# Kernel optimization log

Measured on AMD Instinct MI355X. Metric: run time of the kernel, lower is better.

## Reference

```python
import jax, jax.numpy as jnp
import numpy as np

N = 50000      # node_num
DIN = 128      # input_dim
DH = 128       # hidden_dim
DE = 128       # embedding_dim
DD = 128       # decoder_dim
NE = 800000    # num edges (before self loops)
B = 4096       # drug pairs
EPS = 1e-5


def setup_inputs() -> dict:
    key = jax.random.key(0)
    ks = jax.random.split(key, 16)
    x = jax.random.normal(ks[0], (N, DIN), jnp.float32)
    edge_index = jax.random.randint(ks[1], (2, NE), 0, N, dtype=jnp.int32)
    drug_index = jax.random.randint(ks[2], (B, 2), 0, N, dtype=jnp.int32)
    s = 0.05  # weight scale for numerical sanity
    return {
        "x": x,
        "edge_index": edge_index,
        "drug_index": drug_index,
        "w1": jax.random.normal(ks[3], (DIN, DH), jnp.float32) * s,
        "b1": jnp.zeros((DH,), jnp.float32),
        "w2": jax.random.normal(ks[4], (DH, DH), jnp.float32) * s,
        "b2": jnp.zeros((DH,), jnp.float32),
        "w3": jax.random.normal(ks[5], (DH, DE), jnp.float32) * s,
        "b3": jnp.zeros((DE,), jnp.float32),
        "g1": jnp.ones((DH,), jnp.float32), "be1": jnp.zeros((DH,), jnp.float32),
        "g2": jnp.ones((DH,), jnp.float32), "be2": jnp.zeros((DH,), jnp.float32),
        "g3": jnp.ones((DE,), jnp.float32), "be3": jnp.zeros((DE,), jnp.float32),
        "p1": jax.random.normal(ks[6], (DE, DD), jnp.float32) * s,
        "p2": jax.random.normal(ks[7], (DD, DD), jnp.float32) * s,
    }


def gcn_conv(x, row, col, W, b):
    # row/col already include self loops; PyG: message from row (source), aggregated at col (target)
    n = x.shape[0]
    h = x @ W + b                                   # linear first, as in GCNConv.forward
    deg = jnp.zeros((n,), h.dtype).at[col].add(1.0)  # degree(col) incl. self loops -> >= 1
    dis = deg ** -0.5
    norm = dis[row] * dis[col]                      # [E+N]
    msg = norm[:, None] * h[row]                    # [E+N, d] gather
    return jax.ops.segment_sum(msg, col, num_segments=n)  # scatter-add


def batch_norm(x, gamma, beta):
    m = jnp.mean(x, axis=0)
    v = jnp.mean((x - m) ** 2, axis=0)  # biased var, as torch BatchNorm training
    return (x - m) * jax.lax.rsqrt(v + EPS) * gamma + beta


def leaky(x):
    return jnp.where(x >= 0, x, 0.1 * x)  # LeakyReLU(0.1)


def reference(x, edge_index, drug_index, w1, b1, w2, b2, w3, b3,
              g1, be1, g2, be2, g3, be3, p1, p2):
    n = x.shape[0]
    self_loop = jnp.arange(n, dtype=edge_index.dtype)
    row = jnp.concatenate([edge_index[0], self_loop])
    col = jnp.concatenate([edge_index[1], self_loop])

    h = leaky(batch_norm(gcn_conv(x, row, col, w1, b1), g1, be1))
    h = leaky(batch_norm(gcn_conv(h, row, col, w2, b2), g2, be2))
    h = leaky(batch_norm(gcn_conv(h, row, col, w3, b3), g3, be3))

    di = drug_index.reshape(-1, 2)
    a = h[di[:, 0] - 1]  # [B, DE] (1-based indices; -1 wraps like torch negative index)
    bb = h[di[:, 1] - 1]  # [B, DE]
    t = a @ p1 @ p2 @ p1.T            # [B, DE] bilinear decode, batched
    ypred = jnp.sum(t * bb, axis=1, keepdims=True)  # [B, 1]
    return ypred
```

## Files before the change

kernel.cpp:

```cpp
#include <hip/hip_runtime.h>

#define PAD 64
#define NSLOT 64

__global__ void init_kernel(int* __restrict__ cnt, int n) {
  int i = blockIdx.x * blockDim.x + threadIdx.x;
  int stride = gridDim.x * blockDim.x;
  for (int j = i; j < n; j += stride) cnt[j] = 0;
}

__global__ void fillcsr_kernel(const int* __restrict__ row, const int* __restrict__ col,
                               int* __restrict__ cnt, int* __restrict__ csr, int ne,
                               float* __restrict__ stats, int nstat) {
  int gid = blockIdx.x * blockDim.x + threadIdx.x;
  int stride = gridDim.x * blockDim.x;
  for (int j = gid; j < nstat; j += stride) stats[j] = 0.f;
  if (gid < ne) {
    int d = col[gid];
    int p = atomicAdd(&cnt[d], 1);
    if (p < PAD) csr[d * PAD + p] = row[gid];
  }
}

__global__ __launch_bounds__(256, 4) void gemm_kernel(
    const float* __restrict__ A, const float* __restrict__ W, const float* __restrict__ bias,
    float* __restrict__ out, int n, float invN,
    const float* __restrict__ bn_sum, const float* __restrict__ bn_sq,
    const float* __restrict__ bn_g, const float* __restrict__ bn_b, int use_bn,
    const int* __restrict__ cnt) {
  __shared__ float Ws[32 * 128];
  __shared__ float xs[32 * 128];
  __shared__ float bnsc[128], bnsh[128];
  int tid = threadIdx.x;
  if (tid < 128) {
    if (use_bn) {
      float s = 0.f, q = 0.f;
      for (int r2 = 0; r2 < NSLOT; ++r2) { s += bn_sum[r2 * 128 + tid]; q += bn_sq[r2 * 128 + tid]; }
      float m = s * invN;
      float var = q * invN - m * m;
      float rs = rsqrtf(var + 1e-5f);
      float sc = rs * bn_g[tid];
      bnsc[tid] = sc;
      bnsh[tid] = bn_b[tid] - m * sc;
    } else {
      bnsc[tid] = 1.f; bnsh[tid] = 0.f;
    }
  }
  int base = blockIdx.x * 128;
  int tx = tid & 15, ty = tid >> 4;
  int c0 = tx * 4, r0 = ty * 4;
  int r = tid & 127;
  int row_s = base + r;
  int hf = tid >> 7;
  int kw = tid >> 5;
  int c4 = tid & 31;
  const float4* Arow = (const float4*)(A + (size_t)row_s * 128);
  float acc[8][8];
#pragma unroll
  for (int i = 0; i < 8; ++i)
#pragma unroll
    for (int j = 0; j < 8; ++j) acc[i][j] = 0.f;

  for (int kp = 0; kp < 4; ++kp) {
    __syncthreads();
#pragma unroll
    for (int it = 0; it < 4; ++it) {
      int kl = kw + it * 8;
      float4 wv = ((const float4*)(W + (size_t)(kp * 32 + kl) * 128))[c4];
      *(float4*)&Ws[kl * 128 + c4 * 4] = wv;
    }
#pragma unroll
    for (int it = 0; it < 4; ++it) {
      int kbl = hf + it * 2;
      float4 v = make_float4(0.f, 0.f, 0.f, 0.f);
      if (row_s < n) v = Arow[kp * 8 + kbl];
      if (use_bn) {
        int k0 = kp * 32 + kbl * 4;
        float t;
        t = v.x * bnsc[k0 + 0] + bnsh[k0 + 0]; v.x = t >= 0.f ? t : 0.1f * t;
        t = v.y * bnsc[k0 + 1] + bnsh[k0 + 1]; v.y = t >= 0.f ? t : 0.1f * t;
        t = v.z * bnsc[k0 + 2] + bnsh[k0 + 2]; v.z = t >= 0.f ? t : 0.1f * t;
        t = v.w * bnsc[k0 + 3] + bnsh[k0 + 3]; v.w = t >= 0.f ? t : 0.1f * t;
      }
      int kl = kbl * 4;
      xs[(kl + 0) * 128 + r] = v.x;
      xs[(kl + 1) * 128 + r] = v.y;
      xs[(kl + 2) * 128 + r] = v.z;
      xs[(kl + 3) * 128 + r] = v.w;
    }
    __syncthreads();
#pragma unroll 4
    for (int k = 0; k < 32; ++k) {
      float4 a0 = *(const float4*)&xs[k * 128 + r0];
      float4 a1 = *(const float4*)&xs[k * 128 + 64 + r0];
      float4 w0 = *(const float4*)&Ws[k * 128 + c0];
      float4 w1 = *(const float4*)&Ws[k * 128 + 64 + c0];
      float xr[8], wc[8];
      xr[0] = a0.x; xr[1] = a0.y; xr[2] = a0.z; xr[3] = a0.w;
      xr[4] = a1.x; xr[5] = a1.y; xr[6] = a1.z; xr[7] = a1.w;
      wc[0] = w0.x; wc[1] = w0.y; wc[2] = w0.z; wc[3] = w0.w;
      wc[4] = w1.x; wc[5] = w1.y; wc[6] = w1.z; wc[7] = w1.w;
#pragma unroll
      for (int i = 0; i < 8; ++i)
#pragma unroll
        for (int j = 0; j < 8; ++j)
          acc[i][j] = fmaf(xr[i], wc[j], acc[i][j]);
    }
  }
  float bb0[4], bb1[4];
#pragma unroll
  for (int j = 0; j < 4; ++j) { bb0[j] = bias[c0 + j]; bb1[j] = bias[64 + c0 + j]; }
#pragma unroll
  for (int i = 0; i < 8; ++i) {
    int row = base + (i < 4 ? r0 + i : 64 + r0 + (i - 4));
    if (row < n) {
      float rs = rsqrtf((float)(cnt[row] + 1));
      float4 o0, o1;
      o0.x = (acc[i][0] + bb0[0]) * rs; o0.y = (acc[i][1] + bb0[1]) * rs;
      o0.z = (acc[i][2] + bb0[2]) * rs; o0.w = (acc[i][3] + bb0[3]) * rs;
      o1.x = (acc[i][4] + bb1[0]) * rs; o1.y = (acc[i][5] + bb1[1]) * rs;
      o1.z = (acc[i][6] + bb1[2]) * rs; o1.w = (acc[i][7] + bb1[3]) * rs;
      *(float4*)&out[(size_t)row * 128 + c0] = o0;
      *(float4*)&out[(size_t)row * 128 + 64 + c0] = o1;
    }
  }
}

__global__ __launch_bounds__(256) void agg_kernel(const float* __restrict__ z,
                                                  const int* __restrict__ cnt,
                                                  const int* __restrict__ csr,
                                                  float* __restrict__ out,
                                                  float* __restrict__ Ssum,
                                                  float* __restrict__ Ssq,
                                                  int n, int half) {
  __shared__ float bs[4][128], bq[4][128];
  int tid = threadIdx.x;
  int lane = tid & 63;
  int wv = tid >> 6;
  int w = (blockIdx.x * blockDim.x + tid) >> 6;
  float stx = 0.f, sty = 0.f, qtx = 0.f, qty = 0.f;
  if (w < half) {
    int i0 = w, i1 = w + half;
    bool has1 = (i1 < n);
    const float2* __restrict__ h2 = (const float2*)z;
    unsigned off0 = (unsigned)i0 * 64u + (unsigned)lane;
    unsigned off1 = (unsigned)i1 * 64u + (unsigned)lane;
    float2 self0 = h2[off0];
    float2 self1 = has1 ? h2[off1] : make_float2(0.f, 0.f);
    int c0r = cnt[i0];
    int c1r = has1 ? cnt[i1] : 0;
    float d0 = rsqrtf((float)(c0r + 1));
    float d1 = rsqrtf((float)(c1r + 1));
    int e0 = c0r > PAD ? PAD : c0r;
    int e1 = c1r > PAD ? PAD : c1r;
    const int* __restrict__ lp0 = csr + (size_t)i0 * PAD;
    const int* __restrict__ lp1 = csr + (size_t)i1 * PAD;
    float s0x = self0.x, s0y = self0.y;
    float s1x = self1.x, s1y = self1.y;
    int my0 = (lane < e0) ? lp0[lane] : 0;
    int my1 = (lane < e1) ? lp1[lane] : 0;
    int p0 = 0, p1 = 0;
    while (p0 + 8 <= e0 && p1 + 8 <= e1) {
      float2 v0[8], v1[8];
#pragma unroll
      for (int u = 0; u < 8; ++u) { int s = __shfl(my0, p0 + u, 64); v0[u] = h2[(unsigned)s * 64u + (unsigned)lane]; }
#pragma unroll
      for (int u = 0; u < 8; ++u) { int s = __shfl(my1, p1 + u, 64); v1[u] = h2[(unsigned)s * 64u + (unsigned)lane]; }
#pragma unroll
      for (int u = 0; u < 8; ++u) {
        s0x += v0[u].x; s0y += v0[u].y;
        s1x += v1[u].x; s1y += v1[u].y;
      }
      p0 += 8; p1 += 8;
    }
    for (; p0 + 8 <= e0; p0 += 8) {
      float2 v[8];
#pragma unroll
      for (int u = 0; u < 8; ++u) { int s = __shfl(my0, p0 + u, 64); v[u] = h2[(unsigned)s * 64u + (unsigned)lane]; }
#pragma unroll
      for (int u = 0; u < 8; ++u) { s0x += v[u].x; s0y += v[u].y; }
    }
    for (; p0 + 4 <= e0; p0 += 4) {
      float2 v[4];
#pragma unroll
      for (int u = 0; u < 4; ++u) { int s = __shfl(my0, p0 + u, 64); v[u] = h2[(unsigned)s * 64u + (unsigned)lane]; }
#pragma unroll
      for (int u = 0; u < 4; ++u) { s0x += v[u].x; s0y += v[u].y; }
    }
    for (; p0 < e0; ++p0) {
      int s = __shfl(my0, p0, 64);
      float2 v = h2[(unsigned)s * 64u + (unsigned)lane];
      s0x += v.x; s0y += v.y;
    }
    for (; p1 + 8 <= e1; p1 += 8) {
      float2 v[8];
#pragma unroll
      for (int u = 0; u < 8; ++u) { int s = __shfl(my1, p1 + u, 64); v[u] = h2[(unsigned)s * 64u + (unsigned)lane]; }
#pragma unroll
      for (int u = 0; u < 8; ++u) { s1x += v[u].x; s1y += v[u].y; }
    }
    for (; p1 + 4 <= e1; p1 += 4) {
      float2 v[4];
#pragma unroll
      for (int u = 0; u < 4; ++u) { int s = __shfl(my1, p1 + u, 64); v[u] = h2[(unsigned)s * 64u + (unsigned)lane]; }
#pragma unroll
      for (int u = 0; u < 4; ++u) { s1x += v[u].x; s1y += v[u].y; }
    }
    for (; p1 < e1; ++p1) {
      int s = __shfl(my1, p1, 64);
      float2 v = h2[(unsigned)s * 64u + (unsigned)lane];
      s1x += v.x; s1y += v.y;
    }
    float2 o0; o0.x = d0 * s0x; o0.y = d0 * s0y;
    ((float2*)out)[off0] = o0;
    stx += o0.x; qtx = fmaf(o0.x, o0.x, qtx);
    sty += o0.y; qty = fmaf(o0.y, o0.y, qty);
    if (has1) {
      float2 o1; o1.x = d1 * s1x; o1.y = d1 * s1y;
      ((float2*)out)[off1] = o1;
      stx += o1.x; qtx = fmaf(o1.x, o1.x, qtx);
      sty += o1.y; qty = fmaf(o1.y, o1.y, qty);
    }
  }
  bs[wv][2 * lane] = stx;     bs[wv][2 * lane + 1] = sty;
  bq[wv][2 * lane] = qtx;     bq[wv][2 * lane + 1] = qty;
  __syncthreads();
  if (tid < 128) {
    float s = bs[0][tid] + bs[1][tid] + bs[2][tid] + bs[3][tid];
    float q = bq[0][tid] + bq[1][tid] + bq[2][tid] + bq[3][tid];
    int slot = (blockIdx.x & (NSLOT - 1)) * 128 + tid;
    atomicAdd(&Ssum[slot], s);
    atomicAdd(&Ssq[slot], q);
  }
}

__global__ __launch_bounds__(128) void bilinear_m_kernel(const float* __restrict__ p1,
                                                         const float* __restrict__ p2,
                                                         float* __restrict__ M2) {
  __shared__ float Bs[128 * 129];
  __shared__ float rr[128];
  __shared__ float tmp[128];
  int i = blockIdx.x, t = threadIdx.x;
  rr[t] = p1[i * 128 + t];
  const float4* p24 = (const float4*)p2;
#pragma unroll 8
  for (int it = 0; it < 32; ++it) {
    int f4 = t + 128 * it;
    int k = f4 >> 5, c = f4 & 31;
    float4 v = p24[f4];
    float* d = &Bs[k * 129 + c * 4];
    d[0] = v.x; d[1] = v.y; d[2] = v.z; d[3] = v.w;
  }
  __syncthreads();
  float a0 = 0.f;
#pragma unroll 8
  for (int k = 0; k < 128; ++k) a0 = fmaf(rr[k], Bs[k * 129 + t], a0);
  __syncthreads();
  tmp[t] = a0;
  const float4* p14 = (const float4*)p1;
#pragma unroll 8
  for (int it = 0; it < 32; ++it) {
    int f4 = t + 128 * it;
    int k = f4 >> 5, c = f4 & 31;
    float4 v = p14[f4];
    float* d = &Bs[k * 129 + c * 4];
    d[0] = v.x; d[1] = v.y; d[2] = v.z; d[3] = v.w;
  }
  __syncthreads();
  float a1 = 0.f;
#pragma unroll 8
  for (int l = 0; l < 128; ++l) a1 = fmaf(tmp[l], Bs[t * 129 + l], a1);
  M2[i * 128 + t] = a1;
}

__global__ __launch_bounds__(256) void decoder_kernel(
    const float* __restrict__ h, const int* __restrict__ di, const float* __restrict__ M,
    const float* __restrict__ bn_sum, const float* __restrict__ bn_sq,
    const float* __restrict__ bn_g, const float* __restrict__ bn_b,
    float* __restrict__ out, int npairs, int n, float invN) {
  __shared__ float Ms[128 * 128];
  __shared__ float sc[128], sh[128];
  int tid = threadIdx.x;
  if (tid < 128) {
    float s = 0.f, q = 0.f;
    for (int r2 = 0; r2 < NSLOT; ++r2) { s += bn_sum[r2 * 128 + tid]; q += bn_sq[r2 * 128 + tid]; }
    float m = s * invN;
    float var = q * invN - m * m;
    float rs = rsqrtf(var + 1e-5f);
    float scv = rs * bn_g[tid];
    sc[tid] = scv;
    sh[tid] = bn_b[tid] - m * scv;
  }
  for (int t = tid; t < 4096; t += 256) ((float4*)Ms)[t] = ((const float4*)M)[t];
  __syncthreads();
  int lane = tid & 63, wv = tid >> 6;
  int wid = blockIdx.x * 4 + wv;
  int nw = gridDim.x * 4;
  for (int k = wid; k < npairs; k += nw) {
    int ia = di[2 * k] - 1;     if (ia < 0) ia += n;
    int ib = di[2 * k + 1] - 1; if (ib < 0) ib += n;
    const float2* ap2 = (const float2*)(h + (size_t)ia * 128);
    const float* bp = h + (size_t)ib * 128;
    float2 a2 = ap2[lane];
    float ax = a2.x * sc[2 * lane] + sh[2 * lane];         ax = ax >= 0.f ? ax : 0.1f * ax;
    float ay = a2.y * sc[2 * lane + 1] + sh[2 * lane + 1]; ay = ay >= 0.f ? ay : 0.1f * ay;
    float u0 = 0.f, u1 = 0.f;
#pragma unroll 8
    for (int i2 = 0; i2 < 64; ++i2) {
      float avx = __shfl(ax, i2, 64);
      float avy = __shfl(ay, i2, 64);
      int i = 2 * i2;
      u0 = fmaf(avx, Ms[i * 128 + lane], u0);
      u1 = fmaf(avx, Ms[i * 128 + 64 + lane], u1);
      u0 = fmaf(avy, Ms[(i + 1) * 128 + lane], u0);
      u1 = fmaf(avy, Ms[(i + 1) * 128 + 64 + lane], u1);
    }
    float b0 = bp[lane] * sc[lane] + sh[lane];                b0 = b0 >= 0.f ? b0 : 0.1f * b0;
    float b1 = bp[lane + 64] * sc[lane + 64] + sh[lane + 64]; b1 = b1 >= 0.f ? b1 : 0.1f * b1;
    float part = u0 * b0 + u1 * b1;
#pragma unroll
    for (int o = 32; o; o >>= 1) part += __shfl_down(part, o, 64);
    if (lane == 0) out[k] = part;
  }
}

extern "C" void kernel_launch(void* const* d_in, const int* in_sizes, int n_in,
                              void* d_out, int out_size, void* d_ws, size_t ws_size,
                              hipStream_t stream) {
  const float* x   = (const float*)d_in[0];
  const int*   ei  = (const int*)d_in[1];
  const int*   dri = (const int*)d_in[2];
  const float* w1  = (const float*)d_in[3];
  const float* b1  = (const float*)d_in[4];
  const float* w2  = (const float*)d_in[5];
  const float* b2  = (const float*)d_in[6];
  const float* w3  = (const float*)d_in[7];
  const float* b3  = (const float*)d_in[8];
  const float* g1  = (const float*)d_in[9];
  const float* be1 = (const float*)d_in[10];
  const float* g2  = (const float*)d_in[11];
  const float* be2 = (const float*)d_in[12];
  const float* g3  = (const float*)d_in[13];
  const float* be3 = (const float*)d_in[14];
  const float* p1  = (const float*)d_in[15];
  const float* p2  = (const float*)d_in[16];
  float* out = (float*)d_out;

  int n  = in_sizes[0] / 128;
  int ne = in_sizes[1] / 2;
  int np = in_sizes[2] / 2;
  const int* erow = ei;
  const int* ecol = ei + ne;

  size_t o = 0;
  char* wsb = (char*)d_ws;
  auto alloc = [&](size_t bytes) { void* p = wsb + o; o += (bytes + 255) & ~255ull; return p; };
  float* T1   = (float*)alloc((size_t)n * 128 * 4);
  float* T2   = (float*)alloc((size_t)n * 128 * 4);
  int*   csr  = (int*)alloc((size_t)n * PAD * 4);
  int*   cnt  = (int*)alloc((size_t)n * 4);
  int nstat = 6 * NSLOT * 128;
  float* stats = (float*)alloc((size_t)nstat * 4);
  float* M2   = (float*)alloc(128 * 128 * 4);
  float* Ssum1 = stats;
  float* Ssq1  = stats + 1 * NSLOT * 128;
  float* Ssum2 = stats + 2 * NSLOT * 128;
  float* Ssq2  = stats + 3 * NSLOT * 128;
  float* Ssum3 = stats + 4 * NSLOT * 128;
  float* Ssq3  = stats + 5 * NSLOT * 128;

  float invN = 1.0f / (float)n;
  int eb = (ne + 255) / 256;
  int gb = (n + 127) / 128;
  int half = (n + 1) / 2;
  int ab = (half + 3) / 4;

  init_kernel<<<256, 256, 0, stream>>>(cnt, n);
  fillcsr_kernel<<<eb, 256, 0, stream>>>(erow, ecol, cnt, csr, ne, stats, nstat);

  gemm_kernel<<<gb, 256, 0, stream>>>(x, w1, b1, T1, n, invN, nullptr, nullptr, nullptr, nullptr, 0, cnt);
  agg_kernel<<<ab, 256, 0, stream>>>(T1, cnt, csr, T2, Ssum1, Ssq1, n, half);

  gemm_kernel<<<gb, 256, 0, stream>>>(T2, w2, b2, T1, n, invN, Ssum1, Ssq1, g1, be1, 1, cnt);
  agg_kernel<<<ab, 256, 0, stream>>>(T1, cnt, csr, T2, Ssum2, Ssq2, n, half);

  gemm_kernel<<<gb, 256, 0, stream>>>(T2, w3, b3, T1, n, invN, Ssum2, Ssq2, g2, be2, 1, cnt);
  agg_kernel<<<ab, 256, 0, stream>>>(T1, cnt, csr, T2, Ssum3, Ssq3, n, half);

  bilinear_m_kernel<<<128, 128, 0, stream>>>(p1, p2, M2);
  decoder_kernel<<<256, 256, 0, stream>>>(T2, dri, M2, Ssum3, Ssq3, g3, be3, out, np, n, invN);
}
```

Measured before the change: 373.1 us.

## Fuse whole GCN pipeline into one persistent cooperative kernel with grid syncs

Replaces the chain of separate launches (init, CSR fill, three gemm/aggregate pairs, bilinear matrix, decoder) with a single cooperative persistent kernel that separates phases with grid-wide syncs. Tiles and warps are looped over grid-stride. The bilinear matrix product is computed on spare blocks overlapped with the CSR build and first GEMM. The goal is to remove launch overhead and inter-kernel gaps. The costs are grid.sync overhead, fewer resident blocks than the original grids, and a decoder that now reads M2 from global memory instead of shared.

```diff
diff --git a/kernel.cpp b/kernel.cpp
--- a/kernel.cpp
+++ b/kernel.cpp
@@ -1,36 +1,26 @@
 #include <hip/hip_runtime.h>
+#include <hip/hip_cooperative_groups.h>
+
+namespace cg = cooperative_groups;
 
 #define PAD 64
 #define NSLOT 64
-
-__global__ void init_kernel(int* __restrict__ cnt, int n) {
-  int i = blockIdx.x * blockDim.x + threadIdx.x;
-  int stride = gridDim.x * blockDim.x;
-  for (int j = i; j < n; j += stride) cnt[j] = 0;
-}
-
-__global__ void fillcsr_kernel(const int* __restrict__ row, const int* __restrict__ col,
-                               int* __restrict__ cnt, int* __restrict__ csr, int ne,
-                               float* __restrict__ stats, int nstat) {
-  int gid = blockIdx.x * blockDim.x + threadIdx.x;
-  int stride = gridDim.x * blockDim.x;
-  for (int j = gid; j < nstat; j += stride) stats[j] = 0.f;
-  if (gid < ne) {
-    int d = col[gid];
-    int p = atomicAdd(&cnt[d], 1);
-    if (p < PAD) csr[d * PAD + p] = row[gid];
-  }
-}
-
-__global__ __launch_bounds__(256, 4) void gemm_kernel(
-    const float* __restrict__ A, const float* __restrict__ W, const float* __restrict__ bias,
-    float* __restrict__ out, int n, float invN,
-    const float* __restrict__ bn_sum, const float* __restrict__ bn_sq,
-    const float* __restrict__ bn_g, const float* __restrict__ bn_b, int use_bn,
-    const int* __restrict__ cnt) {
-  __shared__ float Ws[32 * 128];
-  __shared__ float xs[32 * 128];
-  __shared__ float bnsc[128], bnsh[128];
+#define NTHR 256
+
+#define SM_FLOATS 8448
+
+
+__device__ void gemm_phase(const float* __restrict__ A, const float* __restrict__ W,
+                           const float* __restrict__ bias, float* __restrict__ out,
+                           int n, float invN,
+                           const float* __restrict__ bn_sum, const float* __restrict__ bn_sq,
+                           const float* __restrict__ bn_g, const float* __restrict__ bn_b,
+                           int use_bn, const int* __restrict__ cnt,
+                           float* sm, int bid, int nwork) {
+  float* Ws = sm;
+  float* xs = sm + 4096;
+  float* bnsc = sm + 8192;
+  float* bnsh = sm + 8320;
   int tid = threadIdx.x;
   if (tid < 128) {
     if (use_bn) {
@@ -46,103 +36,104 @@
       bnsc[tid] = 1.f; bnsh[tid] = 0.f;
     }
   }
-  int base = blockIdx.x * 128;
+  int ntiles = (n + 127) >> 7;
   int tx = tid & 15, ty = tid >> 4;
   int c0 = tx * 4, r0 = ty * 4;
   int r = tid & 127;
-  int row_s = base + r;
   int hf = tid >> 7;
   int kw = tid >> 5;
   int c4 = tid & 31;
-  const float4* Arow = (const float4*)(A + (size_t)row_s * 128);
-  float acc[8][8];
-#pragma unroll
-  for (int i = 0; i < 8; ++i)
-#pragma unroll
-    for (int j = 0; j < 8; ++j) acc[i][j] = 0.f;
-
-  for (int kp = 0; kp < 4; ++kp) {
-    __syncthreads();
-#pragma unroll
-    for (int it = 0; it < 4; ++it) {
-      int kl = kw + it * 8;
-      float4 wv = ((const float4*)(W + (size_t)(kp * 32 + kl) * 128))[c4];
-      *(float4*)&Ws[kl * 128 + c4 * 4] = wv;
-    }
-#pragma unroll
-    for (int it = 0; it < 4; ++it) {
-      int kbl = hf + it * 2;
-      float4 v = make_float4(0.f, 0.f, 0.f, 0.f);
-      if (row_s < n) v = Arow[kp * 8 + kbl];
-      if (use_bn) {
-        int k0 = kp * 32 + kbl * 4;
-        float t;
-        t = v.x * bnsc[k0 + 0] + bnsh[k0 + 0]; v.x = t >= 0.f ? t : 0.1f * t;
-        t = v.y * bnsc[k0 + 1] + bnsh[k0 + 1]; v.y = t >= 0.f ? t : 0.1f * t;
-        t = v.z * bnsc[k0 + 2] + bnsh[k0 + 2]; v.z = t >= 0.f ? t : 0.1f * t;
-        t = v.w * bnsc[k0 + 3] + bnsh[k0 + 3]; v.w = t >= 0.f ? t : 0.1f * t;
-      }
-      int kl = kbl * 4;
-      xs[(kl + 0) * 128 + r] = v.x;
-      xs[(kl + 1) * 128 + r] = v.y;
-      xs[(kl + 2) * 128 + r] = v.z;
-      xs[(kl + 3) * 128 + r] = v.w;
-    }
-    __syncthreads();
+  for (int tile = bid; tile < ntiles; tile += nwork) {
+    int base = tile << 7;
+    int row_s = base + r;
+    const float4* Arow = (const float4*)(A + (size_t)row_s * 128);
+    float acc[8][8];
+#pragma unroll
+    for (int i = 0; i < 8; ++i)
+#pragma unroll
+      for (int j = 0; j < 8; ++j) acc[i][j] = 0.f;
+    for (int kp = 0; kp < 4; ++kp) {
+      __syncthreads();
+#pragma unroll
+      for (int it = 0; it < 4; ++it) {
+        int kl = kw + it * 8;
+        float4 wv = ((const float4*)(W + (size_t)(kp * 32 + kl) * 128))[c4];
+        *(float4*)&Ws[kl * 128 + c4 * 4] = wv;
+      }
+#pragma unroll
+      for (int it = 0; it < 4; ++it) {
+        int kbl = hf + it * 2;
+        float4 v = make_float4(0.f, 0.f, 0.f, 0.f);
+        if (row_s < n) v = Arow[kp * 8 + kbl];
+        if (use_bn) {
+          int k0 = kp * 32 + kbl * 4;
+          float t;
+          t = v.x * bnsc[k0 + 0] + bnsh[k0 + 0]; v.x = t >= 0.f ? t : 0.1f * t;
+          t = v.y * bnsc[k0 + 1] + bnsh[k0 + 1]; v.y = t >= 0.f ? t : 0.1f * t;
+          t = v.z * bnsc[k0 + 2] + bnsh[k0 + 2]; v.z = t >= 0.f ? t : 0.1f * t;
+          t = v.w * bnsc[k0 + 3] + bnsh[k0 + 3]; v.w = t >= 0.f ? t : 0.1f * t;
+        }
+        int kl = kbl * 4;
+        xs[(kl + 0) * 128 + r] = v.x;
+        xs[(kl + 1) * 128 + r] = v.y;
+        xs[(kl + 2) * 128 + r] = v.z;
+        xs[(kl + 3) * 128 + r] = v.w;
+      }
+      __syncthreads();
 #pragma unroll 4
-    for (int k = 0; k < 32; ++k) {
-      float4 a0 = *(const float4*)&xs[k * 128 + r0];
-      float4 a1 = *(const float4*)&xs[k * 128 + 64 + r0];
-      float4 w0 = *(const float4*)&Ws[k * 128 + c0];
-      float4 w1 = *(const float4*)&Ws[k * 128 + 64 + c0];
-      float xr[8], wc[8];
-      xr[0] = a0.x; xr[1] = a0.y; xr[2] = a0.z; xr[3] = a0.w;
-      xr[4] = a1.x; xr[5] = a1.y; xr[6] = a1.z; xr[7] = a1.w;
-      wc[0] = w0.x; wc[1] = w0.y; wc[2] = w0.z; wc[3] = w0.w;
-      wc[4] = w1.x; wc[5] = w1.y; wc[6] = w1.z; wc[7] = w1.w;
-#pragma unroll
-      for (int i = 0; i < 8; ++i)
-#pragma unroll
-        for (int j = 0; j < 8; ++j)
-          acc[i][j] = fmaf(xr[i], wc[j], acc[i][j]);
-    }
-  }
-  float bb0[4], bb1[4];
-#pragma unroll
-  for (int j = 0; j < 4; ++j) { bb0[j] = bias[c0 + j]; bb1[j] = bias[64 + c0 + j]; }
-#pragma unroll
-  for (int i = 0; i < 8; ++i) {
-    int row = base + (i < 4 ? r0 + i : 64 + r0 + (i - 4));
-    if (row < n) {
-      float rs = rsqrtf((float)(cnt[row] + 1));
-      float4 o0, o1;
-      o0.x = (acc[i][0] + bb0[0]) * rs; o0.y = (acc[i][1] + bb0[1]) * rs;
-      o0.z = (acc[i][2] + bb0[2]) * rs; o0.w = (acc[i][3] + bb0[3]) * rs;
-      o1.x = (acc[i][4] + bb1[0]) * rs; o1.y = (acc[i][5] + bb1[1]) * rs;
-      o1.z = (acc[i][6] + bb1[2]) * rs; o1.w = (acc[i][7] + bb1[3]) * rs;
-      *(float4*)&out[(size_t)row * 128 + c0] = o0;
-      *(float4*)&out[(size_t)row * 128 + 64 + c0] = o1;
-    }
-  }
-}
-
-__global__ __launch_bounds__(256) void agg_kernel(const float* __restrict__ z,
-                                                  const int* __restrict__ cnt,
-                                                  const int* __restrict__ csr,
-                                                  float* __restrict__ out,
-                                                  float* __restrict__ Ssum,
-                                                  float* __restrict__ Ssq,
-                                                  int n, int half) {
-  __shared__ float bs[4][128], bq[4][128];
+      for (int k = 0; k < 32; ++k) {
+        float4 a0 = *(const float4*)&xs[k * 128 + r0];
+        float4 a1 = *(const float4*)&xs[k * 128 + 64 + r0];
+        float4 w0 = *(const float4*)&Ws[k * 128 + c0];
+        float4 w1 = *(const float4*)&Ws[k * 128 + 64 + c0];
+        float xr[8], wc[8];
+        xr[0] = a0.x; xr[1] = a0.y; xr[2] = a0.z; xr[3] = a0.w;
+        xr[4] = a1.x; xr[5] = a1.y; xr[6] = a1.z; xr[7] = a1.w;
+        wc[0] = w0.x; wc[1] = w0.y; wc[2] = w0.z; wc[3] = w0.w;
+        wc[4] = w1.x; wc[5] = w1.y; wc[6] = w1.z; wc[7] = w1.w;
+#pragma unroll
+        for (int i = 0; i < 8; ++i)
+#pragma unroll
+          for (int j = 0; j < 8; ++j)
+            acc[i][j] = fmaf(xr[i], wc[j], acc[i][j]);
+      }
+    }
+    float bb0[4], bb1[4];
+#pragma unroll
+    for (int j = 0; j < 4; ++j) { bb0[j] = bias[c0 + j]; bb1[j] = bias[64 + c0 + j]; }
+#pragma unroll
+    for (int i = 0; i < 8; ++i) {
+      int row = base + (i < 4 ? r0 + i : 64 + r0 + (i - 4));
+      if (row < n) {
+        float rs = rsqrtf((float)(cnt[row] + 1));
+        float4 o0, o1;
+        o0.x = (acc[i][0] + bb0[0]) * rs; o0.y = (acc[i][1] + bb0[1]) * rs;
+        o0.z = (acc[i][2] + bb0[2]) * rs; o0.w = (acc[i][3] + bb0[3]) * rs;
+        o1.x = (acc[i][4] + bb1[0]) * rs; o1.y = (acc[i][5] + bb1[1]) * rs;
+        o1.z = (acc[i][6] + bb1[2]) * rs; o1.w = (acc[i][7] + bb1[3]) * rs;
+        *(float4*)&out[(size_t)row * 128 + c0] = o0;
+        *(float4*)&out[(size_t)row * 128 + 64 + c0] = o1;
+      }
+    }
+  }
+}
+
+__device__ void agg_phase(const float* __restrict__ z, const int* __restrict__ cnt,
+                          const int* __restrict__ csr, float* __restrict__ out,
+                          float* __restrict__ Ssum, float* __restrict__ Ssq,
+                          int n, int half, float* sm) {
+  float* bs = sm;
+  float* bq = sm + 512;
   int tid = threadIdx.x;
   int lane = tid & 63;
   int wv = tid >> 6;
-  int w = (blockIdx.x * blockDim.x + tid) >> 6;
+  int gwv = (blockIdx.x * blockDim.x + tid) >> 6;
+  int nwv = (gridDim.x * blockDim.x) >> 6;
+  const float2* __restrict__ h2 = (const float2*)z;
   float stx = 0.f, sty = 0.f, qtx = 0.f, qty = 0.f;
-  if (w < half) {
+  for (int w = gwv; w < half; w += nwv) {
     int i0 = w, i1 = w + half;
     bool has1 = (i1 < n);
-    const float2* __restrict__ h2 = (const float2*)z;
     unsigned off0 = (unsigned)i0 * 64u + (unsigned)lane;
     unsigned off1 = (unsigned)i1 * 64u + (unsigned)lane;
     float2 self0 = h2[off0];
@@ -222,16 +213,208 @@
       sty += o1.y; qty = fmaf(o1.y, o1.y, qty);
     }
   }
-  bs[wv][2 * lane] = stx;     bs[wv][2 * lane + 1] = sty;
-  bq[wv][2 * lane] = qtx;     bq[wv][2 * lane + 1] = qty;
+  __syncthreads();
+  bs[wv * 128 + 2 * lane] = stx;  bs[wv * 128 + 2 * lane + 1] = sty;
+  bq[wv * 128 + 2 * lane] = qtx;  bq[wv * 128 + 2 * lane + 1] = qty;
   __syncthreads();
   if (tid < 128) {
-    float s = bs[0][tid] + bs[1][tid] + bs[2][tid] + bs[3][tid];
-    float q = bq[0][tid] + bq[1][tid] + bq[2][tid] + bq[3][tid];
-    int slot = (blockIdx.x & (NSLOT - 1)) * 128 + tid;
+    float s = bs[tid] + bs[128 + tid] + bs[256 + tid] + bs[384 + tid];
+    float q = bq[tid] + bq[128 + tid] + bq[256 + tid] + bq[384 + tid];
+    int slot = ((int)blockIdx.x & (NSLOT - 1)) * 128 + tid;
     atomicAdd(&Ssum[slot], s);
     atomicAdd(&Ssq[slot], q);
   }
+}
+
+__device__ void decoder_phase(const float* __restrict__ h, const int* __restrict__ dri,
+                              const float* __restrict__ M2,
+                              const float* __restrict__ Ssum3, const float* __restrict__ Ssq3,
+                              const float* __restrict__ g3, const float* __restrict__ be3,
+                              float* __restrict__ out, int np, int n, float invN,
+                              float* sm, int gid, int gsz) {
+  float* sc = sm;
+  float* sh = sm + 128;
+  int tid = threadIdx.x;
+  __syncthreads();
+  if (tid < 128) {
+    float s = 0.f, q = 0.f;
+    for (int r2 = 0; r2 < NSLOT; ++r2) { s += Ssum3[r2 * 128 + tid]; q += Ssq3[r2 * 128 + tid]; }
+    float m = s * invN;
+    float var = q * invN - m * m;
+    float rs = rsqrtf(var + 1e-5f);
+    float scv = rs * g3[tid];
+    sc[tid] = scv;
+    sh[tid] = be3[tid] - m * scv;
+  }
+  __syncthreads();
+  int lane = tid & 63;
+  int wvid = gid >> 6;
+  int nwv = gsz >> 6;
+  for (int k = wvid; k < np; k += nwv) {
+    int ia = dri[2 * k] - 1;     if (ia < 0) ia += n;
+    int ib = dri[2 * k + 1] - 1; if (ib < 0) ib += n;
+    const float2* ap2 = (const float2*)(h + (size_t)ia * 128);
+    const float* bp = h + (size_t)ib * 128;
+    float2 a2 = ap2[lane];
+    float ax = a2.x * sc[2 * lane] + sh[2 * lane];         ax = ax >= 0.f ? ax : 0.1f * ax;
+    float ay = a2.y * sc[2 * lane + 1] + sh[2 * lane + 1]; ay = ay >= 0.f ? ay : 0.1f * ay;
+    float u0 = 0.f, u1 = 0.f;
+#pragma unroll 4
+    for (int i2 = 0; i2 < 64; ++i2) {
+      float avx = __shfl(ax, i2, 64);
+      float avy = __shfl(ay, i2, 64);
+      const float* Mr = M2 + (size_t)(2 * i2) * 128;
+      u0 = fmaf(avx, Mr[lane], u0);
+      u1 = fmaf(avx, Mr[64 + lane], u1);
+      u0 = fmaf(avy, Mr[128 + lane], u0);
+      u1 = fmaf(avy, Mr[192 + lane], u1);
+    }
+    float b0 = bp[lane] * sc[lane] + sh[lane];                b0 = b0 >= 0.f ? b0 : 0.1f * b0;
+    float b1 = bp[lane + 64] * sc[lane + 64] + sh[lane + 64]; b1 = b1 >= 0.f ? b1 : 0.1f * b1;
+    float part = u0 * b0 + u1 * b1;
+#pragma unroll
+    for (int o = 32; o; o >>= 1) part += __shfl_down(part, o, 64);
+    if (lane == 0) out[k] = part;
+  }
+}
+
+
+__global__ __launch_bounds__(NTHR, 4) void mega_kernel(
+    const float* __restrict__ x, const int* __restrict__ erow, const int* __restrict__ ecol,
+    const int* __restrict__ dri,
+    const float* __restrict__ w1, const float* __restrict__ b1,
+    const float* __restrict__ w2, const float* __restrict__ b2,
+    const float* __restrict__ w3, const float* __restrict__ b3,
+    const float* __restrict__ g1, const float* __restrict__ be1,
+    const float* __restrict__ g2, const float* __restrict__ be2,
+    const float* __restrict__ g3, const float* __restrict__ be3,
+    const float* __restrict__ p1, const float* __restrict__ p2,
+    float* __restrict__ out,
+    float* __restrict__ T1, float* __restrict__ T2,
+    int* __restrict__ csr, int* __restrict__ cnt, float* __restrict__ stats,
+    float* __restrict__ Mtmp, float* __restrict__ M2,
+    int n, int ne, int np, float invN) {
+  cg::grid_group grid = cg::this_grid();
+  __shared__ float sm[SM_FLOATS];
+  int tid = threadIdx.x;
+  int bid = blockIdx.x;
+  int nb = gridDim.x;
+  int gid = bid * NTHR + tid;
+  int gsz = nb * NTHR;
+  int half = (n + 1) / 2;
+  int nstat = 6 * NSLOT * 128;
+  float* Ssum1 = stats;
+  float* Ssq1  = stats + 1 * NSLOT * 128;
+  float* Ssum2 = stats + 2 * NSLOT * 128;
+  float* Ssq2  = stats + 3 * NSLOT * 128;
+  float* Ssum3 = stats + 4 * NSLOT * 128;
+  float* Ssq3  = stats + 5 * NSLOT * 128;
+  int nwork1 = nb - 128;
+
+  for (int j = gid; j < n; j += gsz) cnt[j] = 0;
+  for (int j = gid; j < nstat; j += gsz) stats[j] = 0.f;
+  grid.sync();
+
+  if (bid < nwork1) {
+    for (int e = bid * NTHR + tid; e < ne; e += nwork1 * NTHR) {
+      int d = ecol[e];
+      int p = atomicAdd(&cnt[d], 1);
+      if (p < PAD) csr[d * PAD + p] = erow[e];
+    }
+  } else {
+    int i = bid - nwork1;
+    if (tid < 128) sm[tid] = p1[i * 128 + tid];
+    __syncthreads();
+    if (tid < 128) {
+      float a0 = 0.f, a1 = 0.f, a2 = 0.f, a3 = 0.f;
+      for (int k = 0; k < 128; k += 4) {
+        a0 = fmaf(sm[k + 0], p2[(k + 0) * 128 + tid], a0);
+        a1 = fmaf(sm[k + 1], p2[(k + 1) * 128 + tid], a1);
+        a2 = fmaf(sm[k + 2], p2[(k + 2) * 128 + tid], a2);
+        a3 = fmaf(sm[k + 3], p2[(k + 3) * 128 + tid], a3);
+      }
+      Mtmp[i * 128 + tid] = (a0 + a1) + (a2 + a3);
+    }
+  }
+  grid.sync();
+
+  if (bid < nwork1) {
+    gemm_phase(x, w1, b1, T1, n, invN, nullptr, nullptr, nullptr, nullptr, 0, cnt, sm, bid, nwork1);
+  } else {
+    int i = bid - nwork1;
+    if (tid < 128) sm[tid] = Mtmp[i * 128 + tid];
+    __syncthreads();
+    if (tid < 128) {
+      const float* pj = p1 + (size_t)tid * 128;
+      float a0 = 0.f, a1 = 0.f, a2 = 0.f, a3 = 0.f;
+      for (int l = 0; l < 128; l += 4) {
+        a0 = fmaf(sm[l + 0], pj[l + 0], a0);
+        a1 = fmaf(sm[l + 1], pj[l + 1], a1);
+        a2 = fmaf(sm[l + 2], pj[l + 2], a2);
+        a3 = fmaf(sm[l + 3], pj[l + 3], a3);
+      }
+      M2[i * 128 + tid] = (a0 + a1) + (a2 + a3);
+    }
+  }
+  grid.sync();
+
+  agg_phase(T1, cnt, csr, T2, Ssum1, Ssq1, n, half, sm);
+  grid.sync();
+
+  gemm_phase(T2, w2, b2, T1, n, invN, Ssum1, Ssq1, g1, be1, 1, cnt, sm, bid, nb);
+  grid.sync();
+
+  agg_phase(T1, cnt, csr, T2, Ssum2, Ssq2, n, half, sm);
+  grid.sync();
+
+  gemm_phase(T2, w3, b3, T1, n, invN, Ssum2, Ssq2, g2, be2, 1, cnt, sm, bid, nb);
+  grid.sync();
+
+  agg_phase(T1, cnt, csr, T2, Ssum3, Ssq3, n, half, sm);
+  grid.sync();
+
+  decoder_phase(T2, dri, M2, Ssum3, Ssq3, g3, be3, out, np, n, invN, sm, gid, gsz);
+}
+
+
+__global__ void init_kernel(int* __restrict__ cnt, int n) {
+  int i = blockIdx.x * blockDim.x + threadIdx.x;
+  int stride = gridDim.x * blockDim.x;
+  for (int j = i; j < n; j += stride) cnt[j] = 0;
+}
+
+__global__ void fillcsr_kernel(const int* __restrict__ row, const int* __restrict__ col,
+                               int* __restrict__ cnt, int* __restrict__ csr, int ne,
+                               float* __restrict__ stats, int nstat) {
+  int gid = blockIdx.x * blockDim.x + threadIdx.x;
+  int stride = gridDim.x * blockDim.x;
+  for (int j = gid; j < nstat; j += stride) stats[j] = 0.f;
+  if (gid < ne) {
+    int d = col[gid];
+    int p = atomicAdd(&cnt[d], 1);
+    if (p < PAD) csr[d * PAD + p] = row[gid];
+  }
+}
+
+__global__ __launch_bounds__(NTHR, 4) void gemm_kernel(
+    const float* __restrict__ A, const float* __restrict__ W, const float* __restrict__ bias,
+    float* __restrict__ out, int n, float invN,
+    const float* __restrict__ bn_sum, const float* __restrict__ bn_sq,
+    const float* __restrict__ bn_g, const float* __restrict__ bn_b, int use_bn,
+    const int* __restrict__ cnt) {
+  __shared__ float sm[SM_FLOATS];
+  gemm_phase(A, W, bias, out, n, invN, bn_sum, bn_sq, bn_g, bn_b, use_bn, cnt, sm, blockIdx.x, gridDim.x);
+}
+
+__global__ __launch_bounds__(NTHR) void agg_kernel(const float* __restrict__ z,
+                                                   const int* __restrict__ cnt,
+                                                   const int* __restrict__ csr,
+                                                   float* __restrict__ out,
+                                                   float* __restrict__ Ssum,
+                                                   float* __restrict__ Ssq,
+                                                   int n, int half) {
+  __shared__ float sm[1024];
+  agg_phase(z, cnt, csr, out, Ssum, Ssq, n, half, sm);
 }
 
 __global__ __launch_bounds__(128) void bilinear_m_kernel(const float* __restrict__ p1,
@@ -273,56 +456,17 @@
   M2[i * 128 + t] = a1;
 }
 
-__global__ __launch_bounds__(256) void decoder_kernel(
-    const float* __restrict__ h, const int* __restrict__ di, const float* __restrict__ M,
-    const float* __restrict__ bn_sum, const float* __restrict__ bn_sq,
-    const float* __restrict__ bn_g, const float* __restrict__ bn_b,
-    float* __restrict__ out, int npairs, int n, float invN) {
-  __shared__ float Ms[128 * 128];
-  __shared__ float sc[128], sh[128];
-  int tid = threadIdx.x;
-  if (tid < 128) {
-    float s = 0.f, q = 0.f;
-    for (int r2 = 0; r2 < NSLOT; ++r2) { s += bn_sum[r2 * 128 + tid]; q += bn_sq[r2 * 128 + tid]; }
-    float m = s * invN;
-    float var = q * invN - m * m;
-    float rs = rsqrtf(var + 1e-5f);
-    float scv = rs * bn_g[tid];
-    sc[tid] = scv;
-    sh[tid] = bn_b[tid] - m * scv;
-  }
-  for (int t = tid; t < 4096; t += 256) ((float4*)Ms)[t] = ((const float4*)M)[t];
-  __syncthreads();
-  int lane = tid & 63, wv = tid >> 6;
-  int wid = blockIdx.x * 4 + wv;
-  int nw = gridDim.x * 4;
-  for (int k = wid; k < npairs; k += nw) {
-    int ia = di[2 * k] - 1;     if (ia < 0) ia += n;
-    int ib = di[2 * k + 1] - 1; if (ib < 0) ib += n;
-    const float2* ap2 = (const float2*)(h + (size_t)ia * 128);
-    const float* bp = h + (size_t)ib * 128;
-    float2 a2 = ap2[lane];
-    float ax = a2.x * sc[2 * lane] + sh[2 * lane];         ax = ax >= 0.f ? ax : 0.1f * ax;
-    float ay = a2.y * sc[2 * lane + 1] + sh[2 * lane + 1]; ay = ay >= 0.f ? ay : 0.1f * ay;
-    float u0 = 0.f, u1 = 0.f;
-#pragma unroll 8
-    for (int i2 = 0; i2 < 64; ++i2) {
-      float avx = __shfl(ax, i2, 64);
-      float avy = __shfl(ay, i2, 64);
-      int i = 2 * i2;
-      u0 = fmaf(avx, Ms[i * 128 + lane], u0);
-      u1 = fmaf(avx, Ms[i * 128 + 64 + lane], u1);
-      u0 = fmaf(avy, Ms[(i + 1) * 128 + lane], u0);
-      u1 = fmaf(avy, Ms[(i + 1) * 128 + 64 + lane], u1);
-    }
-    float b0 = bp[lane] * sc[lane] + sh[lane];                b0 = b0 >= 0.f ? b0 : 0.1f * b0;
-    float b1 = bp[lane + 64] * sc[lane + 64] + sh[lane + 64]; b1 = b1 >= 0.f ? b1 : 0.1f * b1;
-    float part = u0 * b0 + u1 * b1;
-#pragma unroll
-    for (int o = 32; o; o >>= 1) part += __shfl_down(part, o, 64);
-    if (lane == 0) out[k] = part;
-  }
-}
+__global__ __launch_bounds__(NTHR) void decoder_kernel(
+    const float* __restrict__ h, const int* __restrict__ dri, const float* __restrict__ M2,
+    const float* __restrict__ Ssum3, const float* __restrict__ Ssq3,
+    const float* __restrict__ g3, const float* __restrict__ be3,
+    float* __restrict__ out, int np, int n, float invN) {
+  __shared__ float sm[256];
+  int gid = blockIdx.x * blockDim.x + threadIdx.x;
+  int gsz = gridDim.x * blockDim.x;
+  decoder_phase(h, dri, M2, Ssum3, Ssq3, g3, be3, out, np, n, invN, sm, gid, gsz);
+}
+
 
 extern "C" void kernel_launch(void* const* d_in, const int* in_sizes, int n_in,
                               void* d_out, int out_size, void* d_ws, size_t ws_size,
@@ -359,8 +503,8 @@
   float* T2   = (float*)alloc((size_t)n * 128 * 4);
   int*   csr  = (int*)alloc((size_t)n * PAD * 4);
   int*   cnt  = (int*)alloc((size_t)n * 4);
-  int nstat = 6 * NSLOT * 128;
-  float* stats = (float*)alloc((size_t)nstat * 4);
+  float* stats = (float*)alloc((size_t)(6 * NSLOT * 128) * 4);
+  float* Mtmp = (float*)alloc(128 * 128 * 4);
   float* M2   = (float*)alloc(128 * 128 * 4);
   float* Ssum1 = stats;
   float* Ssq1  = stats + 1 * NSLOT * 128;
@@ -370,10 +514,36 @@
   float* Ssq3  = stats + 5 * NSLOT * 128;
 
   float invN = 1.0f / (float)n;
+
+  int dev = 0;
+  hipGetDevice(&dev);
+  int nCU = 0;
+  hipDeviceGetAttribute(&nCU, hipDeviceAttributeMultiprocessorCount, dev);
+  int maxBlocksPerCU = 0;
+  hipOccupancyMaxActiveBlocksPerMultiprocessor(&maxBlocksPerCU, mega_kernel, NTHR, 0);
+  int nblk = maxBlocksPerCU * nCU;
+  if (nblk > 2048) nblk = 2048;
+
+  if (nblk >= 384) {
+    void* kargs[] = {
+      (void*)&x, (void*)&erow, (void*)&ecol, (void*)&dri,
+      (void*)&w1, (void*)&b1, (void*)&w2, (void*)&b2, (void*)&w3, (void*)&b3,
+      (void*)&g1, (void*)&be1, (void*)&g2, (void*)&be2, (void*)&g3, (void*)&be3,
+      (void*)&p1, (void*)&p2, (void*)&out,
+      (void*)&T1, (void*)&T2, (void*)&csr, (void*)&cnt, (void*)&stats,
+      (void*)&Mtmp, (void*)&M2,
+      (void*)&n, (void*)&ne, (void*)&np, (void*)&invN
+    };
+    hipError_t err = hipLaunchCooperativeKernel((void*)mega_kernel, dim3(nblk), dim3(NTHR),
+                                                kargs, 0, stream);
+    if (err == hipSuccess) return;
+  }
+
   int eb = (ne + 255) / 256;
   int gb = (n + 127) / 128;
   int half = (n + 1) / 2;
   int ab = (half + 3) / 4;
+  int nstat = 6 * NSLOT * 128;
 
   init_kernel<<<256, 256, 0, stream>>>(cnt, n);
   fillcsr_kernel<<<eb, 256, 0, stream>>>(erow, ecol, cnt, csr, ne, stats, nstat);
```

Measured after the change: 438.1 us. 1.17x slower.
